# Kernel tuning notes

Hardware: AMD Instinct MI355X
Metric: run time of the kernel (lower is better)

## Reference

```python
import jax, jax.numpy as jnp
import numpy as np

N_EMBD = 1024  # C; source scales scores by C**-0.5 (n_embd, not head_size)


def setup_inputs() -> dict:
    key = jax.random.key(0)
    kx, kk, kq, kv = jax.random.split(key, 4)
    B, T, C, H = 8, 2048, N_EMBD, 64
    x = jax.random.normal(kx, (B, T, C), dtype=jnp.float32)
    Wk = jax.random.normal(kk, (C, H), dtype=jnp.float32) * (C ** -0.5)
    Wq = jax.random.normal(kq, (C, H), dtype=jnp.float32) * (C ** -0.5)
    Wv = jax.random.normal(kv, (C, H), dtype=jnp.float32) * (C ** -0.5)
    return {"x": x, "Wk": Wk, "Wq": Wq, "Wv": Wv}


def reference(x, Wk, Wq, Wv):
    B, T, C = x.shape
    k = jnp.einsum('btc,ch->bth', x, Wk)
    q = jnp.einsum('btc,ch->bth', x, Wq)
    v = jnp.einsum('btc,ch->bth', x, Wv)
    # scores scaled by C**-0.5 (faithful to source, which uses n_embd not head_size)
    wei = jnp.einsum('bth,bsh->bts', q, k) * (C ** -0.5)  # [B,T,T]
    causal = jnp.tril(jnp.ones((T, T), dtype=bool))
    wei = jnp.where(causal, wei, -jnp.inf)
    wei = jax.nn.softmax(wei, axis=-1)
    # dropout is identity in eval mode
    out = jnp.einsum('bts,bsh->bth', wei, v)
    return out
```

## Files before the change

### kernel.cpp

```cpp
#include <hip/hip_runtime.h>


#define B_ 8
#define T_ 2048
#define C_ 1024
#define H_ 64
#define BTH (B_ * T_ * H_)

typedef unsigned short u16;
typedef float f32x4 __attribute__((ext_vector_type(4)));
typedef __bf16 bf16x8 __attribute__((ext_vector_type(8)));
#define AS1 __attribute__((address_space(1)))
#define AS3 __attribute__((address_space(3)))

__device__ __forceinline__ u16 f2bf(float f) {
  union { float f; unsigned u; } c; c.f = f;
  unsigned u = c.u;
  return (u16)((u + 0x7FFFu + ((u >> 16) & 1u)) >> 16);
}

__device__ __forceinline__ bf16x8 cvt8(const float4 a, const float4 b) {
  bf16x8 r;
  r[0] = (__bf16)a.x; r[1] = (__bf16)a.y; r[2] = (__bf16)a.z; r[3] = (__bf16)a.w;
  r[4] = (__bf16)b.x; r[5] = (__bf16)b.y; r[6] = (__bf16)b.z; r[7] = (__bf16)b.w;
  return r;
}

__global__ __launch_bounds__(256)
void wpack(const float* __restrict__ Wk, const float* __restrict__ Wq,
           const float* __restrict__ Wv, u16* __restrict__ Wct) {
  const int g  = blockIdx.x;
  const int k0 = blockIdx.y * 64;
  const float* __restrict__ W = (g == 0) ? Wk : (g == 1) ? Wq : Wv;
#pragma unroll
  for (int it = 0; it < 16; ++it) {
    const int idx = it * 256 + threadIdx.x;
    const int kk = k0 + (idx >> 6), h = idx & 63;
    Wct[(size_t)(g * 64 + h) * C_ + kk] = f2bf(W[(size_t)kk * H_ + h]);
  }
}

__global__ __launch_bounds__(256)
void qkv_gemm(const float* __restrict__ x, const u16* __restrict__ Wct,
              u16* __restrict__ ws) {
  __shared__ u16 As[32 * 128];
  const int tid  = threadIdx.x;
  const int wave = tid >> 6, lane = tid & 63;
  const int l15 = lane & 15, quad = lane >> 4;
  const int r0 = blockIdx.x * 32;
  const int srow = tid >> 3, sseg = tid & 7;
  const float* __restrict__ xsrc = x + (size_t)(r0 + srow) * C_ + sseg * 16;
  u16* const wdst0 = As + srow * 128 + ((2 * sseg)     ^ (srow & 15)) * 8;
  u16* const wdst1 = As + srow * 128 + ((2 * sseg + 1) ^ (srow & 15)) * 8;
  const u16* __restrict__ wp = Wct + (size_t)(wave * 48 + l15) * C_ + quad * 8;
  const u16* const ard0 = As + l15 * 128;
  const u16* const ard1 = As + (16 + l15) * 128;
  const f32x4 z = {0.f, 0.f, 0.f, 0.f};
  f32x4 acc[2][3];
#pragma unroll
  for (int m = 0; m < 2; ++m)
#pragma unroll
    for (int ni = 0; ni < 3; ++ni) acc[m][ni] = z;

#pragma unroll 1
  for (int ks = 0; ks < 8; ++ks) {
    const int k0 = ks * 128;
    float4 xa0 = *(const float4*)(xsrc + k0);
    float4 xa1 = *(const float4*)(xsrc + k0 + 4);
    float4 xa2 = *(const float4*)(xsrc + k0 + 8);
    float4 xa3 = *(const float4*)(xsrc + k0 + 12);
    bf16x8 Bf[3][4];
#pragma unroll
    for (int ni = 0; ni < 3; ++ni)
#pragma unroll
      for (int f = 0; f < 4; ++f)
        Bf[ni][f] = *(const bf16x8*)(wp + (size_t)ni * 16 * C_ + k0 + f * 32);
    __syncthreads();
    *(bf16x8*)wdst0 = cvt8(xa0, xa1);
    *(bf16x8*)wdst1 = cvt8(xa2, xa3);
    __syncthreads();
#pragma unroll
    for (int f = 0; f < 4; ++f) {
      const int co = (((4 * f + quad) ^ l15) * 8);
      const bf16x8 a0 = *(const bf16x8*)(ard0 + co);
      const bf16x8 a1 = *(const bf16x8*)(ard1 + co);
#pragma unroll
      for (int ni = 0; ni < 3; ++ni) {
        acc[0][ni] = __builtin_amdgcn_mfma_f32_16x16x32_bf16(a0, Bf[ni][f], acc[0][ni], 0, 0, 0);
        acc[1][ni] = __builtin_amdgcn_mfma_f32_16x16x32_bf16(a1, Bf[ni][f], acc[1][ni], 0, 0, 0);
      }
    }
  }
  const float SCLL = 0.03125f * 1.44269504088896f;
  const int bb = r0 >> 11;
#pragma unroll
  for (int m = 0; m < 2; ++m) {
    const int rowg = r0 + m * 16;
    const int tb = (rowg & 2047) + quad * 4;
#pragma unroll
    for (int ni = 0; ni < 3; ++ni) {
      const int col = wave * 48 + ni * 16 + l15;
      const int g = col >> 6, h = col & 63;
      f32x4 a = acc[m][ni];
      if (g == 1) { a[0] *= SCLL; a[1] *= SCLL; a[2] *= SCLL; a[3] *= SCLL; }
      if (g < 2) {
        u16* op = ws + (size_t)g * BTH + (size_t)(rowg + quad * 4) * H_ + h;
#pragma unroll
        for (int r = 0; r < 4; ++r) op[(size_t)r * H_] = f2bf(a[r]);
      } else {
        uint2 pk;
        pk.x = (unsigned)f2bf(a[0]) | ((unsigned)f2bf(a[1]) << 16);
        pk.y = (unsigned)f2bf(a[2]) | ((unsigned)f2bf(a[3]) << 16);
        *(uint2*)(ws + (size_t)2 * BTH + (size_t)(bb * H_ + h) * T_ + tb) = pk;
      }
    }
  }
}

__global__ __launch_bounds__(128)
void flash(const u16* __restrict__ ws, float* __restrict__ out) {
  __shared__ u16 Ks[2][64 * 64];
  __shared__ u16 Vs[2][64 * 64];
  __shared__ __bf16 Pt[2][16 * 72];
  const u16* __restrict__ kg = ws;
  const u16* __restrict__ qg = ws + BTH;
  const u16* __restrict__ vt = ws + (size_t)2 * BTH;
  const int b    = blockIdx.y;
  const int j    = 63 - (int)blockIdx.x;
  const int tid  = threadIdx.x;
  const int wv   = tid >> 6;
  const int lane = tid & 63;
  const int l15  = lane & 15, quad = lane >> 4;
  const int qt   = 2 * j + wv;
  const int t0   = qt * 16;
  const int ns   = (2 * j + 5) >> 2;
  const u16* kb0 = kg + (size_t)b * T_ * H_;
  const u16* vb0 = vt + (size_t)b * H_ * T_;
  const int srow = tid >> 3, scp = tid & 7;
  const u16* qrow = qg + ((size_t)(b * T_ + t0 + l15)) * H_ + quad * 8;
  const bf16x8 qf0 = *(const bf16x8*)qrow;
  const bf16x8 qf1 = *(const bf16x8*)(qrow + 32);
  __bf16* pt = &Pt[wv][0];
  const f32x4 z = {0.f, 0.f, 0.f, 0.f};
  f32x4 o[4];
  float lr[4] = {0.f, 0.f, 0.f, 0.f};
#pragma unroll
  for (int hi = 0; hi < 4; ++hi) o[hi] = z;

#pragma unroll
  for (int jj = 0; jj < 4; ++jj) {
    const int row = jj * 16 + srow;
    const int sc  = scp ^ (row & 7);
    __builtin_amdgcn_global_load_lds(
        (const AS1 unsigned*)(kb0 + (size_t)row * H_ + sc * 8),
        (AS3 unsigned*)(&Ks[0][(jj * 128 + tid) * 8]), 16, 0, 0);
    __builtin_amdgcn_global_load_lds(
        (const AS1 unsigned*)(vb0 + (size_t)row * T_ + sc * 8),
        (AS3 unsigned*)(&Vs[0][(jj * 128 + tid) * 8]), 16, 0, 0);
  }
  __syncthreads();

#pragma unroll 1
  for (int st = 0; st < ns; ++st) {
    const int cur = st & 1;
    if (st + 1 < ns) {
      const int s1 = (st + 1) * 64;
#pragma unroll
      for (int jj = 0; jj < 4; ++jj) {
        const int row = jj * 16 + srow;
        const int sc  = scp ^ (row & 7);
        __builtin_amdgcn_global_load_lds(
            (const AS1 unsigned*)(kb0 + (size_t)(s1 + row) * H_ + sc * 8),
            (AS3 unsigned*)(&Ks[cur ^ 1][(jj * 128 + tid) * 8]), 16, 0, 0);
        __builtin_amdgcn_global_load_lds(
            (const AS1 unsigned*)(vb0 + (size_t)row * T_ + s1 + sc * 8),
            (AS3 unsigned*)(&Vs[cur ^ 1][(jj * 128 + tid) * 8]), 16, 0, 0);
      }
    }
    const u16* Kc = &Ks[cur][0];
    const u16* Vc = &Vs[cur][0];
    const int sw = (l15 & 7);
    f32x4 s[4];
#pragma unroll
    for (int ni = 0; ni < 4; ++ni) {
      const u16* kr = Kc + (ni * 16 + l15) * 64;
      const bf16x8 k0 = *(const bf16x8*)(kr + ((quad       ^ sw) * 8));
      const bf16x8 k1 = *(const bf16x8*)(kr + (((4 + quad) ^ sw) * 8));
      s[ni] = __builtin_amdgcn_mfma_f32_16x16x32_bf16(qf0, k0, z, 0, 0, 0);
      s[ni] = __builtin_amdgcn_mfma_f32_16x16x32_bf16(qf1, k1, s[ni], 0, 0, 0);
    }
    if (st == ns - 1) {
      const int s0 = st * 64;
#pragma unroll
      for (int ni = 0; ni < 4; ++ni)
#pragma unroll
        for (int r = 0; r < 4; ++r)
          if (s0 + ni * 16 + l15 > t0 + quad * 4 + r) s[ni][r] = -1e30f;
    }
    float p[4][4];
#pragma unroll
    for (int ni = 0; ni < 4; ++ni)
#pragma unroll
      for (int r = 0; r < 4; ++r) p[ni][r] = __builtin_amdgcn_exp2f(s[ni][r]);
#pragma unroll
    for (int r = 0; r < 4; ++r)
      lr[r] += (p[0][r] + p[1][r]) + (p[2][r] + p[3][r]);
#pragma unroll
    for (int ni = 0; ni < 4; ++ni)
#pragma unroll
      for (int r = 0; r < 4; ++r)
        pt[(quad * 4 + r) * 72 + ni * 16 + l15] = (__bf16)p[ni][r];
    asm volatile("s_waitcnt lgkmcnt(0)" ::: "memory");
    const bf16x8 pa0 = *(const bf16x8*)(pt + l15 * 72 + quad * 8);
    const bf16x8 pa1 = *(const bf16x8*)(pt + l15 * 72 + 32 + quad * 8);
    asm volatile("" ::: "memory");
#pragma unroll
    for (int hi = 0; hi < 4; ++hi) {
      const u16* vr = Vc + (hi * 16 + l15) * 64;
      const bf16x8 v0 = *(const bf16x8*)(vr + ((quad       ^ sw) * 8));
      const bf16x8 v1 = *(const bf16x8*)(vr + (((4 + quad) ^ sw) * 8));
      o[hi] = __builtin_amdgcn_mfma_f32_16x16x32_bf16(pa0, v0, o[hi], 0, 0, 0);
      o[hi] = __builtin_amdgcn_mfma_f32_16x16x32_bf16(pa1, v1, o[hi], 0, 0, 0);
    }
    __syncthreads();
  }
#pragma unroll
  for (int d = 1; d < 16; d <<= 1)
#pragma unroll
    for (int r = 0; r < 4; ++r) lr[r] += __shfl_xor(lr[r], d, 64);
  float* ob = out + ((size_t)b * T_ + t0 + quad * 4) * H_ + l15;
#pragma unroll
  for (int r = 0; r < 4; ++r) {
    const float inv = 1.0f / lr[r];
#pragma unroll
    for (int hi = 0; hi < 4; ++hi)
      ob[(size_t)r * H_ + 16 * hi] = o[hi][r] * inv;
  }
}

extern "C" void kernel_launch(void* const* d_in, const int* in_sizes, int n_in,
                              void* d_out, int out_size, void* d_ws, size_t ws_size,
                              hipStream_t stream) {
  const float* x  = (const float*)d_in[0];
  const float* Wk = (const float*)d_in[1];
  const float* Wq = (const float*)d_in[2];
  const float* Wv = (const float*)d_in[3];
  u16*   ws  = (u16*)d_ws;
  u16*   Wct = ws + (size_t)3 * BTH;
  float* out = (float*)d_out;
  wpack<<<dim3(3, 16), 256, 0, stream>>>(Wk, Wq, Wv, Wct);
  qkv_gemm<<<dim3(512), 256, 0, stream>>>(x, Wct, ws);
  flash<<<dim3(64, B_), 128, 0, stream>>>(ws, out);
}
```

Before: 160.5 us.

## Split causal attention over KV chunks with atomic accumulation, double-buffer QKV GEMM

The flash kernel now splits each query tile's KV range into chunks of up to 8 steps across a third grid dimension. Each chunk atomically adds its unnormalized output and row sums into a pre-zeroed output and a workspace buffer, and a new normalize kernel divides afterwards. This is meant to fix the load imbalance and limited parallelism of long causal rows. The QKV GEMM moves to 512 threads with double-buffered LDS and register prefetch of x, and the weight pack transposes through LDS for coalesced access. The cost is two extra launches, float atomics that make summation order nondeterministic, and extra output traffic; correctness relies on the kernel not tracking a per-row running max.

```diff
diff --git a/kernel.cpp b/kernel.cpp
--- a/kernel.cpp
+++ b/kernel.cpp
@@ -6,6 +6,7 @@
 #define C_ 1024
 #define H_ 64
 #define BTH (B_ * T_ * H_)
+#define LWS_OFF ((size_t)3 * BTH + 192 * 1024)
 
 typedef unsigned short u16;
 typedef float f32x4 __attribute__((ext_vector_type(4)));
@@ -27,98 +28,115 @@
 }
 
 __global__ __launch_bounds__(256)
+void zero_out(float4* __restrict__ out4, float4* __restrict__ l4) {
+  const int i = blockIdx.x * 256 + threadIdx.x;
+  const float4 z = make_float4(0.f, 0.f, 0.f, 0.f);
+  if (i < 262144) out4[i] = z;
+  else            l4[i - 262144] = z;
+}
+
+__global__ __launch_bounds__(256)
 void wpack(const float* __restrict__ Wk, const float* __restrict__ Wq,
            const float* __restrict__ Wv, u16* __restrict__ Wct) {
+  __shared__ float t[64][65];
   const int g  = blockIdx.x;
   const int k0 = blockIdx.y * 64;
   const float* __restrict__ W = (g == 0) ? Wk : (g == 1) ? Wq : Wv;
+  const int c = threadIdx.x & 63, r4 = threadIdx.x >> 6;
 #pragma unroll
   for (int it = 0; it < 16; ++it) {
-    const int idx = it * 256 + threadIdx.x;
-    const int kk = k0 + (idx >> 6), h = idx & 63;
-    Wct[(size_t)(g * 64 + h) * C_ + kk] = f2bf(W[(size_t)kk * H_ + h]);
-  }
-}
-
-__global__ __launch_bounds__(256)
+    const int row = it * 4 + r4;
+    t[row][c] = W[(size_t)(k0 + row) * H_ + c];
+  }
+  __syncthreads();
+#pragma unroll
+  for (int it = 0; it < 16; ++it) {
+    const int hrow = it * 4 + r4;
+    Wct[(size_t)(g * 64 + hrow) * C_ + k0 + c] = f2bf(t[c][hrow]);
+  }
+}
+
+__global__ __launch_bounds__(512)
 void qkv_gemm(const float* __restrict__ x, const u16* __restrict__ Wct,
               u16* __restrict__ ws) {
-  __shared__ u16 As[32 * 128];
+  __shared__ u16 As[2][32 * 128];
   const int tid  = threadIdx.x;
   const int wave = tid >> 6, lane = tid & 63;
   const int l15 = lane & 15, quad = lane >> 4;
+  const int m = wave & 1, ng = wave >> 1;
   const int r0 = blockIdx.x * 32;
-  const int srow = tid >> 3, sseg = tid & 7;
-  const float* __restrict__ xsrc = x + (size_t)(r0 + srow) * C_ + sseg * 16;
-  u16* const wdst0 = As + srow * 128 + ((2 * sseg)     ^ (srow & 15)) * 8;
-  u16* const wdst1 = As + srow * 128 + ((2 * sseg + 1) ^ (srow & 15)) * 8;
-  const u16* __restrict__ wp = Wct + (size_t)(wave * 48 + l15) * C_ + quad * 8;
-  const u16* const ard0 = As + l15 * 128;
-  const u16* const ard1 = As + (16 + l15) * 128;
+  const int srow = tid >> 4, sch = tid & 15;
+  const float* __restrict__ xsrc = x + (size_t)(r0 + srow) * C_ + sch * 8;
+  const int wslot = srow * 128 + (sch ^ (srow & 15)) * 8;
+  const u16* __restrict__ wp = Wct + (size_t)(ng * 48 + l15) * C_ + quad * 8;
+  const int arow = (m * 16 + l15) * 128;
   const f32x4 z = {0.f, 0.f, 0.f, 0.f};
-  f32x4 acc[2][3];
-#pragma unroll
-  for (int m = 0; m < 2; ++m)
-#pragma unroll
-    for (int ni = 0; ni < 3; ++ni) acc[m][ni] = z;
-
-#pragma unroll 1
+  f32x4 acc[3];
+#pragma unroll
+  for (int ni = 0; ni < 3; ++ni) acc[ni] = z;
+
+  float4 xa0 = *(const float4*)(xsrc);
+  float4 xa1 = *(const float4*)(xsrc + 4);
+  *(bf16x8*)(&As[0][wslot]) = cvt8(xa0, xa1);
+  xa0 = *(const float4*)(xsrc + 128);
+  xa1 = *(const float4*)(xsrc + 132);
+  __syncthreads();
+
+#pragma unroll
   for (int ks = 0; ks < 8; ++ks) {
+    const int cur = ks & 1;
     const int k0 = ks * 128;
-    float4 xa0 = *(const float4*)(xsrc + k0);
-    float4 xa1 = *(const float4*)(xsrc + k0 + 4);
-    float4 xa2 = *(const float4*)(xsrc + k0 + 8);
-    float4 xa3 = *(const float4*)(xsrc + k0 + 12);
     bf16x8 Bf[3][4];
 #pragma unroll
     for (int ni = 0; ni < 3; ++ni)
 #pragma unroll
       for (int f = 0; f < 4; ++f)
         Bf[ni][f] = *(const bf16x8*)(wp + (size_t)ni * 16 * C_ + k0 + f * 32);
+    if (ks < 7) *(bf16x8*)(&As[cur ^ 1][wslot]) = cvt8(xa0, xa1);
+    if (ks < 6) {
+      xa0 = *(const float4*)(xsrc + (ks + 2) * 128);
+      xa1 = *(const float4*)(xsrc + (ks + 2) * 128 + 4);
+    }
+#pragma unroll
+    for (int f = 0; f < 4; ++f) {
+      const bf16x8 a = *(const bf16x8*)(&As[cur][arow + (((4 * f + quad) ^ l15) * 8)]);
+#pragma unroll
+      for (int ni = 0; ni < 3; ++ni)
+        acc[ni] = __builtin_amdgcn_mfma_f32_16x16x32_bf16(a, Bf[ni][f], acc[ni], 0, 0, 0);
+    }
     __syncthreads();
-    *(bf16x8*)wdst0 = cvt8(xa0, xa1);
-    *(bf16x8*)wdst1 = cvt8(xa2, xa3);
-    __syncthreads();
-#pragma unroll
-    for (int f = 0; f < 4; ++f) {
-      const int co = (((4 * f + quad) ^ l15) * 8);
-      const bf16x8 a0 = *(const bf16x8*)(ard0 + co);
-      const bf16x8 a1 = *(const bf16x8*)(ard1 + co);
-#pragma unroll
-      for (int ni = 0; ni < 3; ++ni) {
-        acc[0][ni] = __builtin_amdgcn_mfma_f32_16x16x32_bf16(a0, Bf[ni][f], acc[0][ni], 0, 0, 0);
-        acc[1][ni] = __builtin_amdgcn_mfma_f32_16x16x32_bf16(a1, Bf[ni][f], acc[1][ni], 0, 0, 0);
-      }
-    }
   }
   const float SCLL = 0.03125f * 1.44269504088896f;
+  const int rowg = r0 + m * 16;
   const int bb = r0 >> 11;
-#pragma unroll
-  for (int m = 0; m < 2; ++m) {
-    const int rowg = r0 + m * 16;
-    const int tb = (rowg & 2047) + quad * 4;
-#pragma unroll
-    for (int ni = 0; ni < 3; ++ni) {
-      const int col = wave * 48 + ni * 16 + l15;
-      const int g = col >> 6, h = col & 63;
-      f32x4 a = acc[m][ni];
-      if (g == 1) { a[0] *= SCLL; a[1] *= SCLL; a[2] *= SCLL; a[3] *= SCLL; }
-      if (g < 2) {
-        u16* op = ws + (size_t)g * BTH + (size_t)(rowg + quad * 4) * H_ + h;
-#pragma unroll
-        for (int r = 0; r < 4; ++r) op[(size_t)r * H_] = f2bf(a[r]);
-      } else {
-        uint2 pk;
-        pk.x = (unsigned)f2bf(a[0]) | ((unsigned)f2bf(a[1]) << 16);
-        pk.y = (unsigned)f2bf(a[2]) | ((unsigned)f2bf(a[3]) << 16);
-        *(uint2*)(ws + (size_t)2 * BTH + (size_t)(bb * H_ + h) * T_ + tb) = pk;
-      }
+  const int tb = (rowg & 2047) + quad * 4;
+#pragma unroll
+  for (int ni = 0; ni < 3; ++ni) {
+    const int col = ng * 48 + ni * 16 + l15;
+    const int g = col >> 6, h = col & 63;
+    f32x4 a = acc[ni];
+    if (g == 1) { a[0] *= SCLL; a[1] *= SCLL; a[2] *= SCLL; a[3] *= SCLL; }
+    if (g < 2) {
+      u16* op = ws + (size_t)g * BTH + (size_t)(rowg + quad * 4) * H_ + h;
+#pragma unroll
+      for (int r = 0; r < 4; ++r) op[(size_t)r * H_] = f2bf(a[r]);
+    } else {
+      uint2 pk;
+      pk.x = (unsigned)f2bf(a[0]) | ((unsigned)f2bf(a[1]) << 16);
+      pk.y = (unsigned)f2bf(a[2]) | ((unsigned)f2bf(a[3]) << 16);
+      *(uint2*)(ws + (size_t)2 * BTH + (size_t)(bb * H_ + h) * T_ + tb) = pk;
     }
   }
 }
 
 __global__ __launch_bounds__(128)
-void flash(const u16* __restrict__ ws, float* __restrict__ out) {
+void flash(const u16* __restrict__ ws, float* __restrict__ out, float* __restrict__ Lws) {
+  const int j  = blockIdx.x;
+  const int ns = (2 * j + 5) >> 2;
+  const int c  = blockIdx.z;
+  if (c * 8 >= ns) return;
+  const int st0   = c * 8;
+  const int stEnd = min(st0 + 8, ns);
   __shared__ u16 Ks[2][64 * 64];
   __shared__ u16 Vs[2][64 * 64];
   __shared__ __bf16 Pt[2][16 * 72];
@@ -126,14 +144,12 @@
   const u16* __restrict__ qg = ws + BTH;
   const u16* __restrict__ vt = ws + (size_t)2 * BTH;
   const int b    = blockIdx.y;
-  const int j    = 63 - (int)blockIdx.x;
   const int tid  = threadIdx.x;
   const int wv   = tid >> 6;
   const int lane = tid & 63;
   const int l15  = lane & 15, quad = lane >> 4;
   const int qt   = 2 * j + wv;
   const int t0   = qt * 16;
-  const int ns   = (2 * j + 5) >> 2;
   const u16* kb0 = kg + (size_t)b * T_ * H_;
   const u16* vb0 = vt + (size_t)b * H_ * T_;
   const int srow = tid >> 3, scp = tid & 7;
@@ -147,23 +163,26 @@
 #pragma unroll
   for (int hi = 0; hi < 4; ++hi) o[hi] = z;
 
-#pragma unroll
-  for (int jj = 0; jj < 4; ++jj) {
-    const int row = jj * 16 + srow;
-    const int sc  = scp ^ (row & 7);
-    __builtin_amdgcn_global_load_lds(
-        (const AS1 unsigned*)(kb0 + (size_t)row * H_ + sc * 8),
-        (AS3 unsigned*)(&Ks[0][(jj * 128 + tid) * 8]), 16, 0, 0);
-    __builtin_amdgcn_global_load_lds(
-        (const AS1 unsigned*)(vb0 + (size_t)row * T_ + sc * 8),
-        (AS3 unsigned*)(&Vs[0][(jj * 128 + tid) * 8]), 16, 0, 0);
+  {
+    const int s0 = st0 * 64;
+#pragma unroll
+    for (int jj = 0; jj < 4; ++jj) {
+      const int row = jj * 16 + srow;
+      const int sc  = scp ^ (row & 7);
+      __builtin_amdgcn_global_load_lds(
+          (const AS1 unsigned*)(kb0 + (size_t)(s0 + row) * H_ + sc * 8),
+          (AS3 unsigned*)(&Ks[0][(jj * 128 + tid) * 8]), 16, 0, 0);
+      __builtin_amdgcn_global_load_lds(
+          (const AS1 unsigned*)(vb0 + (size_t)row * T_ + s0 + sc * 8),
+          (AS3 unsigned*)(&Vs[0][(jj * 128 + tid) * 8]), 16, 0, 0);
+    }
   }
   __syncthreads();
 
 #pragma unroll 1
-  for (int st = 0; st < ns; ++st) {
-    const int cur = st & 1;
-    if (st + 1 < ns) {
+  for (int st = st0; st < stEnd; ++st) {
+    const int cur = (st - st0) & 1;
+    if (st + 1 < stEnd) {
       const int s1 = (st + 1) * 64;
 #pragma unroll
       for (int jj = 0; jj < 4; ++jj) {
@@ -230,12 +249,25 @@
     for (int r = 0; r < 4; ++r) lr[r] += __shfl_xor(lr[r], d, 64);
   float* ob = out + ((size_t)b * T_ + t0 + quad * 4) * H_ + l15;
 #pragma unroll
-  for (int r = 0; r < 4; ++r) {
-    const float inv = 1.0f / lr[r];
+  for (int r = 0; r < 4; ++r)
 #pragma unroll
     for (int hi = 0; hi < 4; ++hi)
-      ob[(size_t)r * H_ + 16 * hi] = o[hi][r] * inv;
-  }
+      atomicAdd(ob + (size_t)r * H_ + 16 * hi, o[hi][r]);
+  if (l15 == 0) {
+#pragma unroll
+    for (int r = 0; r < 4; ++r)
+      atomicAdd(Lws + (size_t)b * T_ + t0 + quad * 4 + r, lr[r]);
+  }
+}
+
+__global__ __launch_bounds__(256)
+void normalize(float4* __restrict__ out4, const float* __restrict__ Lws) {
+  const int row = blockIdx.x * 16 + (threadIdx.x >> 4);
+  const int c4  = threadIdx.x & 15;
+  const float inv = 1.0f / Lws[row];
+  float4 v = out4[(size_t)row * 16 + c4];
+  v.x *= inv; v.y *= inv; v.z *= inv; v.w *= inv;
+  out4[(size_t)row * 16 + c4] = v;
 }
 
 extern "C" void kernel_launch(void* const* d_in, const int* in_sizes, int n_in,
@@ -247,8 +279,11 @@
   const float* Wv = (const float*)d_in[3];
   u16*   ws  = (u16*)d_ws;
   u16*   Wct = ws + (size_t)3 * BTH;
+  float* Lws = (float*)(ws + LWS_OFF);
   float* out = (float*)d_out;
+  zero_out<<<dim3(1040), 256, 0, stream>>>((float4*)out, (float4*)Lws);
   wpack<<<dim3(3, 16), 256, 0, stream>>>(Wk, Wq, Wv, Wct);
-  qkv_gemm<<<dim3(512), 256, 0, stream>>>(x, Wct, ws);
-  flash<<<dim3(64, B_), 128, 0, stream>>>(ws, out);
-}
+  qkv_gemm<<<dim3(512), 512, 0, stream>>>(x, Wct, ws);
+  flash<<<dim3(64, B_, 4), 128, 0, stream>>>(ws, out, Lws);
+  normalize<<<dim3(1024), 256, 0, stream>>>((float4*)out, Lws);
+}
```

Result: slower. 170.5 us (+6.2%).
